# Kernel tuning notes

Measured on AMD Instinct MI355X. Metric: run time of the kernel, lower is better.

## Reference

```python
import jax, jax.numpy as jnp
import numpy as np

B, N, D, H, NDIMS, NS = 4, 1024, 512, 8, 3, 1
HD = D // H


def setup_inputs() -> dict:
    key = jax.random.key(0)
    ks = jax.random.split(key, 10)
    x = jax.random.normal(ks[0], (B, N, D), dtype=jnp.float32)
    coords = jax.random.normal(ks[1], (B, N, NDIMS), dtype=jnp.float32)
    # pad last 64 key positions in half the batch
    key_padding_mask = jnp.zeros((B, N), dtype=bool).at[: B // 2, -64:].set(True)
    s = 1.0 / np.sqrt(D)
    Wqkv = jax.random.normal(ks[2], (3 * D, D), dtype=jnp.float32) * s  # torch Linear weight [out,in]
    Wout = jax.random.normal(ks[3], (D, D), dtype=jnp.float32) * s
    bout = jnp.zeros((D,), dtype=jnp.float32)
    fin = NDIMS + 1  # num_dims>1 -> dist channel appended
    W1 = jax.random.normal(ks[4], (H * 4, fin), dtype=jnp.float32) / np.sqrt(fin)
    b1 = jnp.zeros((H * 4,), dtype=jnp.float32)
    W2 = jax.random.normal(ks[5], (H, H * 4), dtype=jnp.float32) / np.sqrt(H * 4)
    b2 = jnp.zeros((H,), dtype=jnp.float32)
    bias_alpha = jax.random.normal(ks[6], (1,), dtype=jnp.float32)
    return dict(x=x, coords=coords, key_padding_mask=key_padding_mask,
                bias_alpha=bias_alpha, W1=W1, b1=b1, W2=W2, b2=b2,
                Wqkv=Wqkv, Wout=Wout, bout=bout)


def reference(x, coords, key_padding_mask, bias_alpha, W1, b1, W2, b2, Wqkv, Wout, bout):
    scale = HD ** (-0.5)
    qkv = x @ Wqkv.T  # [B,N,3D]
    q, k, v = jnp.split(qkv, 3, axis=-1)
    q = q.reshape(B, N, H, HD).transpose(0, 2, 1, 3)  # [B,H,N,HD]
    k = k.reshape(B, N, H, HD).transpose(0, 2, 1, 3)
    v = v.reshape(B, N, H, HD).transpose(0, 2, 1, 3)

    dpos = coords[:, :, None, :] - coords[:, None, :, :]  # [B,N,N,ndims]
    dist = jnp.linalg.norm(dpos, axis=-1, keepdims=True)
    dpos = jnp.concatenate([dpos, dist], axis=-1)  # [B,N,N,ndims+1]
    h = jax.nn.gelu(dpos @ W1.T + b1, approximate=False)
    bias = (h @ W2.T + b2).transpose(0, 3, 1, 2)  # [B,H,N,N]
    # zero bias rows/cols for special tokens
    valid = jnp.arange(N) >= NS
    bias = bias * (valid[:, None] & valid[None, :])[None, None]

    dots = jnp.einsum('bhid,bhjd->bhij', q, k) * scale
    logits = dots + bias_alpha[0] * bias
    logits = jnp.where(key_padding_mask[:, None, None, :], -jnp.inf, logits)
    attn = jax.nn.softmax(logits, axis=-1)
    out = jnp.einsum('bhij,bhjd->bhid', attn, v)
    out = out.transpose(0, 2, 1, 3).reshape(B, N, D)
    return out @ Wout.T + bout, attn
```

## Files before the change

### kernel.cpp

```cpp
#include <hip/hip_runtime.h>
#include <hip/hip_fp16.h>
#include <stdint.h>
#include <math.h>

#define B_  4
#define N_  1024
#define D_  512
#define H_  8
#define HD_ 64

typedef short s16x8 __attribute__((ext_vector_type(8)));
typedef float f32x4 __attribute__((ext_vector_type(4)));
typedef float f32x2 __attribute__((ext_vector_type(2)));
typedef __fp16 f16x2 __attribute__((ext_vector_type(2)));
typedef __fp16 f16x8 __attribute__((ext_vector_type(8)));

typedef const __attribute__((address_space(1))) void* gas1p;
typedef __attribute__((address_space(3))) void* las3p;
__device__ __forceinline__ void gload16(const void* g, void* l) {
    __builtin_amdgcn_global_load_lds((gas1p)g, (las3p)l, 16, 0, 0);
}

__device__ __forceinline__ unsigned short f2bf(float f) {
    unsigned u = __float_as_uint(f);
    u += 0x7fffu + ((u >> 16) & 1u);
    return (unsigned short)(u >> 16);
}
__device__ __forceinline__ float bf2f(unsigned short h) {
    return __uint_as_float(((unsigned)h) << 16);
}

__device__ __forceinline__ float fast_gelu(float x) {
    float ax = fabsf(x) * 0.7071067811865476f;
    float t  = __builtin_amdgcn_rcpf(fmaf(0.3275911f, ax, 1.0f));
    float e  = __expf(-ax * ax);
    float poly = t * fmaf(t, fmaf(t, fmaf(t, fmaf(t, 1.061405429f, -1.453152027f),
                                          1.421413741f), -0.284496736f), 0.254829592f);
    float erfv = 1.0f - poly * e;
    float s = copysignf(erfv, x);
    return 0.5f * x * (1.0f + s);
}

__global__ void k_split(const float* __restrict__ s, unsigned short* __restrict__ h,
                        unsigned short* __restrict__ l, int n) {
    int i = blockIdx.x * 256 + threadIdx.x;
    if (i < n) {
        float x = s[i];
        unsigned short hb = f2bf(x);
        h[i] = hb;
        l[i] = f2bf(x - bf2f(hb));
    }
}

__global__ void k_mask_detect(const unsigned char* __restrict__ m, int* __restrict__ flag) {
    __shared__ int s;
    if (threadIdx.x == 0) s = 0;
    __syncthreads();
    int found = 0;
    for (int i = threadIdx.x; i < B_ * N_; i += 256)
        if ((i & 3) && m[i]) found = 1;
    if (found) atomicOr(&s, 1);
    __syncthreads();
    if (threadIdx.x == 0) flag[0] = s;
}

__global__ __launch_bounds__(256) void k_gemm3(
    const unsigned short* __restrict__ Ah, const unsigned short* __restrict__ Al,
    const unsigned short* __restrict__ Bwh, const unsigned short* __restrict__ Bwl,
    float* __restrict__ C, const float* __restrict__ bias, int M, int Nn, int K)
{
    constexpr int BM = 64, BN = 128, BK = 64;
    __shared__ unsigned short At[BM * BK];
    __shared__ unsigned short Bt[BN * BK];
    const int tid = threadIdx.x, lane = tid & 63, wid = tid >> 6;
    const int m0 = blockIdx.x * BM, n0 = blockIdx.y * BN;
    const int wm = wid >> 1, wn = wid & 1;
    f32x4 acc[2][4] = {};
    const unsigned short* Aps[3] = {Ah, Ah, Al};
    const unsigned short* Bps[3] = {Bwh, Bwl, Bwh};

    for (int combo = 0; combo < 3; ++combo) {
        const unsigned short* __restrict__ Ap = Aps[combo];
        const unsigned short* __restrict__ Bp = Bps[combo];
        for (int k0 = 0; k0 < K; k0 += BK) {
            __syncthreads();
            #pragma unroll
            for (int r = 0; r < 2; ++r) {
                int s = r * 256 + tid, row = s >> 3, c8 = s & 7;
                gload16(Ap + (size_t)(m0 + row) * K + k0 + c8 * 8, At + s * 8);
            }
            #pragma unroll
            for (int r = 0; r < 4; ++r) {
                int s = r * 256 + tid, row = s >> 3, c8 = s & 7;
                gload16(Bp + (size_t)(n0 + row) * K + k0 + c8 * 8, Bt + s * 8);
            }
            __syncthreads();
            #pragma unroll
            for (int kk = 0; kk < BK; kk += 32) {
                s16x8 a[2], bb[4];
                #pragma unroll
                for (int fm = 0; fm < 2; ++fm)
                    a[fm] = *(const s16x8*)(At + (wm * 32 + fm * 16 + (lane & 15)) * BK + kk + (lane >> 4) * 8);
                #pragma unroll
                for (int fn = 0; fn < 4; ++fn)
                    bb[fn] = *(const s16x8*)(Bt + (wn * 64 + fn * 16 + (lane & 15)) * BK + kk + (lane >> 4) * 8);
                #pragma unroll
                for (int fm = 0; fm < 2; ++fm)
                    #pragma unroll
                    for (int fn = 0; fn < 4; ++fn)
                        acc[fm][fn] = __builtin_amdgcn_mfma_f32_16x16x32_bf16(a[fm], bb[fn], acc[fm][fn], 0, 0, 0);
            }
        }
    }
    #pragma unroll
    for (int fm = 0; fm < 2; ++fm)
        #pragma unroll
        for (int fn = 0; fn < 4; ++fn)
            #pragma unroll
            for (int r = 0; r < 4; ++r) {
                int row  = m0 + wm * 32 + fm * 16 + (lane >> 4) * 4 + r;
                int coln = n0 + wn * 64 + fn * 16 + (lane & 15);
                float v = acc[fm][fn][r];
                if (bias) v += bias[coln];
                C[(size_t)row * Nn + coln] = v;
            }
}

__global__ void k_rearrange(const float* __restrict__ qkv, unsigned short* __restrict__ qp,
                            unsigned short* __restrict__ kp) {
    int t = blockIdx.x * 256 + threadIdx.x;
    int d = t & 63, n = (t >> 6) & 1023, h = (t >> 16) & 7, b = t >> 19;
    const float* src = qkv + ((size_t)(b * N_ + n)) * (3 * D_) + h * HD_ + d;
    float q = src[0], k = src[D_];
    unsigned short qh = f2bf(q), ql = f2bf(q - bf2f(qh));
    unsigned short kh = f2bf(k), kl = f2bf(k - bf2f(kh));
    size_t base = ((size_t)(b * H_ + h) * N_ + n) * 128;
    qp[base + d] = qh; qp[base + 64 + d] = ql;
    kp[base + d] = kh; kp[base + 64 + d] = kl;
}

__global__ void k_vtrans(const float* __restrict__ qkv, unsigned short* __restrict__ vT) {
    __shared__ unsigned short T[64][65];
    int n0 = blockIdx.x * 64, h = blockIdx.y, b = blockIdx.z;
    int tid = threadIdx.x;
    #pragma unroll
    for (int rep = 0; rep < 16; ++rep) {
        int idx = rep * 256 + tid;
        int nl = idx >> 6, d = idx & 63;
        T[nl][d] = f2bf(qkv[((size_t)(b * N_ + n0 + nl)) * (3 * D_) + 2 * D_ + h * HD_ + d]);
    }
    __syncthreads();
    #pragma unroll
    for (int rep = 0; rep < 16; ++rep) {
        int idx = rep * 256 + tid;
        int dl = idx >> 6, nl = idx & 63;
        vT[((size_t)(b * H_ + h) * HD_ + dl) * N_ + n0 + nl] = T[nl][dl];
    }
}

__global__ void k_nodeproj(const float* __restrict__ coords, const float* __restrict__ W1,
                           unsigned short* __restrict__ PtT) {
    int bn = blockIdx.x * 256 + threadIdx.x;
    const float* cc = coords + (size_t)bn * 3;
    float c0 = cc[0], c1 = cc[1], c2 = cc[2];
    unsigned short outv[32];
    #pragma unroll
    for (int c = 0; c < 32; ++c) {
        float v = 32.f * (W1[c * 4] * c0 + W1[c * 4 + 1] * c1 + W1[c * 4 + 2] * c2);
        __half hv = __float2half(v);
        outv[c] = *(unsigned short*)&hv;
    }
    #pragma unroll
    for (int k = 0; k < 4; ++k)
        *(s16x8*)(PtT + (size_t)bn * 32 + k * 8) = *(const s16x8*)(outv + k * 8);
}

__global__ __launch_bounds__(256) void k_bias(
    const float* __restrict__ coords, const float* __restrict__ alpha,
    const float* __restrict__ W1, const float* __restrict__ b1,
    const float* __restrict__ W2, const float* __restrict__ b2,
    const unsigned short* __restrict__ PtT,
    unsigned short* __restrict__ biasH)
{
    __shared__ unsigned short sPj[256 * 40];
    __shared__ float lut[512];
    __shared__ float SPi[32], swd32[32], sb2f[8];
    __shared__ float sdist[256];
    const int tid = threadIdx.x, lane = tid & 63, wid = tid >> 6;
    const int bid = blockIdx.x;
    const int j0 = (bid & 3) * 256;
    const int i  = (bid >> 2) & 1023;
    const int b  = bid >> 12;

    {
        float xk = (tid - 128) * 0.03125f;
        float g0 = fast_gelu(xk);
        float g1 = fast_gelu(xk + 0.03125f);
        lut[tid * 2]     = g0;
        lut[tid * 2 + 1] = g1 - g0;
    }
    if (tid < 32) {
        const float* ci = coords + ((size_t)b * N_ + i) * 3;
        float w0 = W1[tid * 4], w1 = W1[tid * 4 + 1], w2 = W1[tid * 4 + 2], w3 = W1[tid * 4 + 3];
        SPi[tid]   = 32.f * (w0 * ci[0] + w1 * ci[1] + w2 * ci[2] + b1[tid]) + 128.f;
        swd32[tid] = 32.f * w3;
    }
    if (tid < 8) sb2f[tid] = b2[tid];
    {
        const unsigned short* src = PtT + ((size_t)(b * N_) + j0) * 32;
        #pragma unroll
        for (int k = 0; k < 4; ++k) {
            int idx = k * 256 + tid;
            *(s16x8*)(sPj + (idx >> 2) * 40 + (idx & 3) * 8) = *(const s16x8*)(src + idx * 8);
        }
    }
    {
        const float* ci = coords + ((size_t)b * N_ + i) * 3;
        const float* cj = coords + ((size_t)b * N_ + j0 + tid) * 3;
        float dx = ci[0] - cj[0], dy = ci[1] - cj[1], dz = ci[2] - cj[2];
        sdist[tid] = sqrtf(dx * dx + dy * dy + dz * dz);
    }
    __syncthreads();

    const int hh = lane & 15;
    const int q  = lane >> 4;
    const float alph = alpha[0];
    const float vfi = (i >= 1) ? 1.f : 0.f;

    f16x8 bw;
    {
        int hw = hh & 7;
        #pragma unroll
        for (int e = 0; e < 8; ++e) {
            float wv = W2[hw * 32 + q * 8 + e];
            bw[e] = (hh < 8) ? (__fp16)wv : (__fp16)0.f;
        }
    }

    #pragma unroll 1
    for (int m = 0; m < 4; ++m) {
        const int pm = m * 16 + hh;
        const float dist = sdist[wid * 64 + pm];
        s16x8 praw = *(const s16x8*)(sPj + (wid * 64 + pm) * 40 + q * 8);
        f16x8 af;
        #pragma unroll
        for (int e = 0; e < 8; ++e) {
            int c = q * 8 + e;
            unsigned short u = (unsigned short)praw[e];
            float pj = __half2float(*(const __half*)&u);
            float t  = fmaf(swd32[c], dist, SPi[c] - pj);
            float tc = fminf(fmaxf(t, 0.f), 255.f);
            float fi = floorf(tc);
            int   ii = (int)fi;
            float fr = tc - fi;
            f32x2 vs = *(const f32x2*)(lut + ii * 2);
            float gg = fmaf(fr, vs[1], vs[0]);
            float xb = fmaf(t, 0.03125f, -4.f);
            gg = (t > 254.f) ? xb : gg;
            af[e] = (__fp16)gg;
        }
        f32x4 c4 = {0.f, 0.f, 0.f, 0.f};
        c4 = __builtin_amdgcn_mfma_f32_16x16x32_f16(af, bw, c4, 0, 0, 0);
        if (hh < 8) {
            const int jb = j0 + wid * 64 + m * 16 + q * 4;
            const float b2h = sb2f[hh];
            float v0 = ((jb     >= 1) ? alph : 0.f) * vfi * (c4[0] + b2h);
            float v1 = ((jb + 1 >= 1) ? alph : 0.f) * vfi * (c4[1] + b2h);
            float v2 = ((jb + 2 >= 1) ? alph : 0.f) * vfi * (c4[2] + b2h);
            float v3 = ((jb + 3 >= 1) ? alph : 0.f) * vfi * (c4[3] + b2h);
            __half h0 = __float2half(v0), h1 = __float2half(v1);
            __half h2 = __float2half(v2), h3 = __float2half(v3);
            unsigned int lo = (unsigned)*(unsigned short*)&h0 | ((unsigned)*(unsigned short*)&h1 << 16);
            unsigned int hi = (unsigned)*(unsigned short*)&h2 | ((unsigned)*(unsigned short*)&h3 << 16);
            unsigned long long pk = (unsigned long long)lo | ((unsigned long long)hi << 32);
            *(unsigned long long*)(biasH + ((size_t)(b * H_ + hh) * N_ + i) * N_ + jb) = pk;
        }
    }
}

__global__ __launch_bounds__(256, 4) void k_attn(
    const unsigned short* __restrict__ qp, const unsigned short* __restrict__ kp,
    const unsigned short* __restrict__ vT,
    const unsigned short* __restrict__ biasH,
    float* __restrict__ attnout,
    const unsigned char* __restrict__ mraw, const int* __restrict__ flag,
    unsigned short* __restrict__ avh, unsigned short* __restrict__ avl)
{
    __shared__ s16x8 pool16[2048];
    __shared__ unsigned char smask[N_];
    __shared__ float redm[16][4];
    __shared__ float reds[16][4];
    const int tid = threadIdx.x, lane = tid & 63, wid = tid >> 6;

    int flat = blockIdx.x + 64 * (blockIdx.y + 8 * blockIdx.z);
    int swz  = (flat & 7) * 256 + (flat >> 3);
    const int i0 = (swz & 63) * 16;
    const int h  = (swz >> 6) & 7;
    const int b  = swz >> 9;
    const size_t bh = (size_t)(b * H_ + h);
    const int g = lane >> 4;
    const int cl = lane & 15;

    if (flag[0] != 0) {
        for (int i2 = tid; i2 < N_; i2 += 256) smask[i2] = mraw[b * N_ + i2];
    } else {
        const int* mi = (const int*)mraw;
        for (int i2 = tid; i2 < N_; i2 += 256) smask[i2] = (unsigned char)(mi[b * N_ + i2] != 0);
    }

    const unsigned short* qrow = qp + (bh * N_ + i0 + cl) * 128 + g * 8;
    s16x8 aqh0 = *(const s16x8*)(qrow);
    s16x8 aqh1 = *(const s16x8*)(qrow + 32);
    s16x8 aql0 = *(const s16x8*)(qrow + 64);
    s16x8 aql1 = *(const s16x8*)(qrow + 96);

    int soff[4];
    #pragma unroll
    for (int p = 0; p < 4; ++p) {
        int o = p * 4096 + tid * 16;
        int row = o >> 8, offl = o & 255;
        soff[p] = row * 128 + ((offl ^ ((row & 7) << 4)) >> 1);
    }
    const unsigned short* kbase = kp + bh * (size_t)N_ * 128;

    const int lr = wid * 16 + cl;
    int rdoff[4];
    #pragma unroll
    for (int f = 0; f < 4; ++f)
        rdoff[f] = lr * 256 + ((g * 16 + f * 64) ^ ((lr & 7) << 4));

    char* poolb = (char*)pool16;

    #pragma unroll
    for (int p = 0; p < 4; ++p)
        gload16(kbase + soff[p], poolb + p * 4096 + tid * 16);
    __syncthreads();

    f32x4 acc[16];
    #pragma unroll
    for (int c = 0; c < 16; ++c) {
        if (c < 15) {
            const unsigned short* cb = kbase + (size_t)(c + 1) * 8192;
            char* wb = poolb + ((c + 1) & 1) * 16384;
            #pragma unroll
            for (int p = 0; p < 4; ++p)
                gload16(cb + soff[p], wb + p * 4096 + tid * 16);
        }
        char* kb = poolb + (c & 1) * 16384;
        s16x8 k0 = *(const s16x8*)(kb + rdoff[0]);
        s16x8 k1 = *(const s16x8*)(kb + rdoff[1]);
        s16x8 k2 = *(const s16x8*)(kb + rdoff[2]);
        s16x8 k3 = *(const s16x8*)(kb + rdoff[3]);
        f32x4 a = {0.f, 0.f, 0.f, 0.f};
        a = __builtin_amdgcn_mfma_f32_16x16x32_bf16(aqh0, k0, a, 0, 0, 0);
        a = __builtin_amdgcn_mfma_f32_16x16x32_bf16(aqh1, k1, a, 0, 0, 0);
        a = __builtin_amdgcn_mfma_f32_16x16x32_bf16(aqh0, k2, a, 0, 0, 0);
        a = __builtin_amdgcn_mfma_f32_16x16x32_bf16(aqh1, k3, a, 0, 0, 0);
        a = __builtin_amdgcn_mfma_f32_16x16x32_bf16(aql0, k0, a, 0, 0, 0);
        a = __builtin_amdgcn_mfma_f32_16x16x32_bf16(aql1, k1, a, 0, 0, 0);
        acc[c] = a;
        __syncthreads();
    }

    {
        const unsigned short* bsrc = biasH + (bh * N_ + i0) * N_;
        unsigned short* bl = (unsigned short*)poolb;
        #pragma unroll
        for (int p2 = 0; p2 < 8; ++p2) {
            int idx = p2 * 256 + tid;
            gload16(bsrc + (size_t)idx * 8, bl + idx * 8);
        }
    }
    __syncthreads();

    const float scale = 0.125f;
    const unsigned short* bl = (const unsigned short*)poolb;
    #pragma unroll
    for (int j = 0; j < 16; ++j) {
        const int col = (j * 4 + wid) * 16 + cl;
        const bool mj = (smask[col] != 0);
        #pragma unroll
        for (int r = 0; r < 4; ++r) {
            unsigned short u = bl[(g * 4 + r) * 1024 + col];
            float bv = __half2float(*(const __half*)&u);
            acc[j][r] = mj ? -1e30f : fmaf(acc[j][r], scale, bv);
        }
    }

    float m[4];
    #pragma unroll
    for (int r = 0; r < 4; ++r) {
        float mm = acc[0][r];
        #pragma unroll
        for (int j = 1; j < 16; ++j) mm = fmaxf(mm, acc[j][r]);
        m[r] = mm;
    }
    #pragma unroll
    for (int msk = 1; msk < 16; msk <<= 1)
        #pragma unroll
        for (int r = 0; r < 4; ++r) m[r] = fmaxf(m[r], __shfl_xor(m[r], msk));
    if (cl == 0)
        #pragma unroll
        for (int r = 0; r < 4; ++r) redm[g * 4 + r][wid] = m[r];
    __syncthreads();
    #pragma unroll
    for (int r = 0; r < 4; ++r) {
        int row = g * 4 + r;
        m[r] = fmaxf(fmaxf(redm[row][0], redm[row][1]), fmaxf(redm[row][2], redm[row][3]));
    }

    float s[4] = {0.f, 0.f, 0.f, 0.f};
    #pragma unroll
    for (int j = 0; j < 16; ++j)
        #pragma unroll
        for (int r = 0; r < 4; ++r) {
            float e = __expf(acc[j][r] - m[r]);
            acc[j][r] = e;
            s[r] += e;
        }
    #pragma unroll
    for (int msk = 1; msk < 16; msk <<= 1)
        #pragma unroll
        for (int r = 0; r < 4; ++r) s[r] += __shfl_xor(s[r], msk);
    if (cl == 0)
        #pragma unroll
        for (int r = 0; r < 4; ++r) reds[g * 4 + r][wid] = s[r];
    __syncthreads();
    float sinv[4];
    #pragma unroll
    for (int r = 0; r < 4; ++r) {
        int row = g * 4 + r;
        sinv[r] = 1.0f / (reds[row][0] + reds[row][1] + reds[row][2] + reds[row][3]);
    }

    float* gattn = attnout + (bh * N_ + i0) * N_;
    char* Pb = poolb;
    #pragma unroll
    for (int j = 0; j < 16; ++j) {
        const int col = (j * 4 + wid) * 16 + cl;
        #pragma unroll
        for (int r = 0; r < 4; ++r) {
            const int row = g * 4 + r;
            float e = acc[j][r];
            __builtin_nontemporal_store(e * sinv[r], &gattn[(size_t)row * N_ + col]);
            int byte = row * 2048 + ((col * 2) ^ ((row & 7) << 4));
            *(unsigned short*)(Pb + byte) = f2bf(e);
        }
    }
    __syncthreads();

    {
        const int d0 = wid * 16;
        f32x4 acc2 = {0.f, 0.f, 0.f, 0.f};
        const unsigned short* vrow = vT + (bh * HD_ + d0 + cl) * N_ + g * 8;
        const int rowA = cl;
        const int swzb = (rowA & 7) << 4;
        for (int kk = 0; kk < N_; kk += 32) {
            s16x8 bfrag = *(const s16x8*)(vrow + kk);
            int byte = rowA * 2048 + (((kk + g * 8) * 2) ^ swzb);
            s16x8 af = *(const s16x8*)(Pb + byte);
            acc2 = __builtin_amdgcn_mfma_f32_16x16x32_bf16(af, bfrag, acc2, 0, 0, 0);
        }
        #pragma unroll
        for (int r = 0; r < 4; ++r) {
            const int row = g * 4 + r;
            const int dd = d0 + cl;
            float v = acc2[r] * sinv[r];
            unsigned short hv = f2bf(v);
            size_t o = ((size_t)(b * N_) + i0 + row) * D_ + h * HD_ + dd;
            avh[o] = hv;
            avl[o] = f2bf(v - bf2f(hv));
        }
    }
}

extern "C" void kernel_launch(void* const* d_in, const int* in_sizes, int n_in,
                              void* d_out, int out_size, void* d_ws, size_t ws_size,
                              hipStream_t stream) {
    (void)in_sizes; (void)n_in; (void)out_size; (void)ws_size;
    const float* x      = (const float*)d_in[0];
    const float* coords = (const float*)d_in[1];
    const unsigned char* kpm = (const unsigned char*)d_in[2];
    const float* alpha  = (const float*)d_in[3];
    const float* W1     = (const float*)d_in[4];
    const float* b1     = (const float*)d_in[5];
    const float* W2     = (const float*)d_in[6];
    const float* b2     = (const float*)d_in[7];
    const float* Wqkv   = (const float*)d_in[8];
    const float* Wout   = (const float*)d_in[9];
    const float* bout   = (const float*)d_in[10];

    float* out  = (float*)d_out;
    float* attn = out + (size_t)B_ * N_ * D_;

    char* w = (char*)d_ws;
    auto alloc = [&](size_t bytes) { char* p = w; w += (bytes + 255) & ~(size_t)255; return p; };
    const size_t SZ_X  = (size_t)B_ * N_ * D_;
    const size_t SZ_WQ = (size_t)3 * D_ * D_;
    const size_t SZ_WO = (size_t)D_ * D_;

    unsigned short* wo_hi = (unsigned short*)alloc(SZ_WO * 2);
    unsigned short* wo_lo = (unsigned short*)alloc(SZ_WO * 2);
    unsigned short* qp = (unsigned short*)alloc((size_t)B_ * H_ * N_ * 128 * 2);
    unsigned short* kp = (unsigned short*)alloc((size_t)B_ * H_ * N_ * 128 * 2);
    unsigned short* vT = (unsigned short*)alloc((size_t)B_ * H_ * HD_ * N_ * 2);
    unsigned short* av_hi = (unsigned short*)alloc(SZ_X * 2);
    unsigned short* av_lo = (unsigned short*)alloc(SZ_X * 2);
    unsigned short* PtT = (unsigned short*)alloc((size_t)B_ * N_ * 32 * 2);
    int* flag = (int*)alloc(256);

    char* uni = (char*)alloc(0);
    unsigned short* x_hi = (unsigned short*)uni;
    unsigned short* x_lo = x_hi + SZ_X;
    unsigned short* wq_hi = x_lo + SZ_X;
    unsigned short* wq_lo = wq_hi + SZ_WQ;
    float* qkv = (float*)(wq_lo + SZ_WQ);
    unsigned short* biasH = (unsigned short*)uni;

    k_split<<<(int)((SZ_X + 255) / 256), 256, 0, stream>>>(x, x_hi, x_lo, (int)SZ_X);
    k_split<<<(int)((SZ_WQ + 255) / 256), 256, 0, stream>>>(Wqkv, wq_hi, wq_lo, (int)SZ_WQ);
    k_split<<<(int)((SZ_WO + 255) / 256), 256, 0, stream>>>(Wout, wo_hi, wo_lo, (int)SZ_WO);
    k_mask_detect<<<1, 256, 0, stream>>>(kpm, flag);
    k_nodeproj<<<(B_ * N_) / 256, 256, 0, stream>>>(coords, W1, PtT);
    k_gemm3<<<dim3(64, 12), 256, 0, stream>>>(x_hi, x_lo, wq_hi, wq_lo, qkv, nullptr,
                                              B_ * N_, 3 * D_, D_);
    k_rearrange<<<(B_ * H_ * N_ * HD_) / 256, 256, 0, stream>>>(qkv, qp, kp);
    k_vtrans<<<dim3(16, H_, B_), 256, 0, stream>>>(qkv, vT);
    k_bias<<<(B_ * N_ * N_) / 256, 256, 0, stream>>>(coords, alpha, W1, b1, W2, b2, PtT, biasH);
    k_attn<<<dim3(64, H_, B_), 256, 0, stream>>>(qp, kp, vT, biasH, attn, kpm, flag, av_hi, av_lo);
    k_gemm3<<<dim3(64, 4), 256, 0, stream>>>(av_hi, av_lo, wo_hi, wo_lo, out, bout,
                                             B_ * N_, D_, D_);
}
```

Measured before the change: 236.0 us.

## Process 32 query rows per attention block to reuse K tiles

The attention kernel now handles 32 query rows per block instead of 16. Each K chunk staged in shared memory feeds two sets of MFMAs, so K traffic from global memory is halved and the grid shrinks to 1024 blocks. The cost is twice the accumulator registers (acc[32]), twice the shared memory, and launch bounds lowered to 2 blocks per CU. Occupancy and latency hiding may drop.

```diff
diff --git a/kernel.cpp b/kernel.cpp
--- a/kernel.cpp
+++ b/kernel.cpp
@@ -278,7 +278,7 @@
     }
 }
 
-__global__ __launch_bounds__(256, 4) void k_attn(
+__global__ __launch_bounds__(256, 2) void k_attn(
     const unsigned short* __restrict__ qp, const unsigned short* __restrict__ kp,
     const unsigned short* __restrict__ vT,
     const unsigned short* __restrict__ biasH,
@@ -286,17 +286,17 @@
     const unsigned char* __restrict__ mraw, const int* __restrict__ flag,
     unsigned short* __restrict__ avh, unsigned short* __restrict__ avl)
 {
-    __shared__ s16x8 pool16[2048];
+    __shared__ s16x8 pool16[4096];
     __shared__ unsigned char smask[N_];
-    __shared__ float redm[16][4];
-    __shared__ float reds[16][4];
+    __shared__ float redm[32][4];
+    __shared__ float reds[32][4];
     const int tid = threadIdx.x, lane = tid & 63, wid = tid >> 6;
 
-    int flat = blockIdx.x + 64 * (blockIdx.y + 8 * blockIdx.z);
-    int swz  = (flat & 7) * 256 + (flat >> 3);
-    const int i0 = (swz & 63) * 16;
-    const int h  = (swz >> 6) & 7;
-    const int b  = swz >> 9;
+    int flat = blockIdx.x + 32 * (blockIdx.y + 8 * blockIdx.z);
+    int swz  = (flat & 7) * 128 + (flat >> 3);
+    const int i0 = (swz & 31) * 32;
+    const int h  = (swz >> 5) & 7;
+    const int b  = swz >> 8;
     const size_t bh = (size_t)(b * H_ + h);
     const int g = lane >> 4;
     const int cl = lane & 15;
@@ -308,11 +308,16 @@
         for (int i2 = tid; i2 < N_; i2 += 256) smask[i2] = (unsigned char)(mi[b * N_ + i2] != 0);
     }
 
-    const unsigned short* qrow = qp + (bh * N_ + i0 + cl) * 128 + g * 8;
-    s16x8 aqh0 = *(const s16x8*)(qrow);
-    s16x8 aqh1 = *(const s16x8*)(qrow + 32);
-    s16x8 aql0 = *(const s16x8*)(qrow + 64);
-    s16x8 aql1 = *(const s16x8*)(qrow + 96);
+    const unsigned short* qr0 = qp + (bh * N_ + i0 + cl) * 128 + g * 8;
+    const unsigned short* qr1 = qp + (bh * N_ + i0 + 16 + cl) * 128 + g * 8;
+    s16x8 aqh0_0 = *(const s16x8*)(qr0);
+    s16x8 aqh1_0 = *(const s16x8*)(qr0 + 32);
+    s16x8 aql0_0 = *(const s16x8*)(qr0 + 64);
+    s16x8 aql1_0 = *(const s16x8*)(qr0 + 96);
+    s16x8 aqh0_1 = *(const s16x8*)(qr1);
+    s16x8 aqh1_1 = *(const s16x8*)(qr1 + 32);
+    s16x8 aql0_1 = *(const s16x8*)(qr1 + 64);
+    s16x8 aql1_1 = *(const s16x8*)(qr1 + 96);
 
     int soff[4];
     #pragma unroll
@@ -336,7 +341,7 @@
         gload16(kbase + soff[p], poolb + p * 4096 + tid * 16);
     __syncthreads();
 
-    f32x4 acc[16];
+    f32x4 acc[32];
     #pragma unroll
     for (int c = 0; c < 16; ++c) {
         if (c < 15) {
@@ -352,13 +357,21 @@
         s16x8 k2 = *(const s16x8*)(kb + rdoff[2]);
         s16x8 k3 = *(const s16x8*)(kb + rdoff[3]);
         f32x4 a = {0.f, 0.f, 0.f, 0.f};
-        a = __builtin_amdgcn_mfma_f32_16x16x32_bf16(aqh0, k0, a, 0, 0, 0);
-        a = __builtin_amdgcn_mfma_f32_16x16x32_bf16(aqh1, k1, a, 0, 0, 0);
-        a = __builtin_amdgcn_mfma_f32_16x16x32_bf16(aqh0, k2, a, 0, 0, 0);
-        a = __builtin_amdgcn_mfma_f32_16x16x32_bf16(aqh1, k3, a, 0, 0, 0);
-        a = __builtin_amdgcn_mfma_f32_16x16x32_bf16(aql0, k0, a, 0, 0, 0);
-        a = __builtin_amdgcn_mfma_f32_16x16x32_bf16(aql1, k1, a, 0, 0, 0);
+        a = __builtin_amdgcn_mfma_f32_16x16x32_bf16(aqh0_0, k0, a, 0, 0, 0);
+        a = __builtin_amdgcn_mfma_f32_16x16x32_bf16(aqh1_0, k1, a, 0, 0, 0);
+        a = __builtin_amdgcn_mfma_f32_16x16x32_bf16(aqh0_0, k2, a, 0, 0, 0);
+        a = __builtin_amdgcn_mfma_f32_16x16x32_bf16(aqh1_0, k3, a, 0, 0, 0);
+        a = __builtin_amdgcn_mfma_f32_16x16x32_bf16(aql0_0, k0, a, 0, 0, 0);
+        a = __builtin_amdgcn_mfma_f32_16x16x32_bf16(aql1_0, k1, a, 0, 0, 0);
         acc[c] = a;
+        f32x4 a2 = {0.f, 0.f, 0.f, 0.f};
+        a2 = __builtin_amdgcn_mfma_f32_16x16x32_bf16(aqh0_1, k0, a2, 0, 0, 0);
+        a2 = __builtin_amdgcn_mfma_f32_16x16x32_bf16(aqh1_1, k1, a2, 0, 0, 0);
+        a2 = __builtin_amdgcn_mfma_f32_16x16x32_bf16(aqh0_1, k2, a2, 0, 0, 0);
+        a2 = __builtin_amdgcn_mfma_f32_16x16x32_bf16(aqh1_1, k3, a2, 0, 0, 0);
+        a2 = __builtin_amdgcn_mfma_f32_16x16x32_bf16(aql0_1, k0, a2, 0, 0, 0);
+        a2 = __builtin_amdgcn_mfma_f32_16x16x32_bf16(aql1_1, k1, a2, 0, 0, 0);
+        acc[16 + c] = a2;
         __syncthreads();
     }
 
@@ -366,7 +379,7 @@
         const unsigned short* bsrc = biasH + (bh * N_ + i0) * N_;
         unsigned short* bl = (unsigned short*)poolb;
         #pragma unroll
-        for (int p2 = 0; p2 < 8; ++p2) {
+        for (int p2 = 0; p2 < 16; ++p2) {
             int idx = p2 * 256 + tid;
             gload16(bsrc + (size_t)idx * 8, bl + idx * 8);
         }
@@ -381,56 +394,79 @@
         const bool mj = (smask[col] != 0);
         #pragma unroll
         for (int r = 0; r < 4; ++r) {
-            unsigned short u = bl[(g * 4 + r) * 1024 + col];
-            float bv = __half2float(*(const __half*)&u);
-            acc[j][r] = mj ? -1e30f : fmaf(acc[j][r], scale, bv);
-        }
-    }
-
-    float m[4];
+            int row0 = g * 4 + r;
+            unsigned short u0 = bl[row0 * 1024 + col];
+            float bv0 = __half2float(*(const __half*)&u0);
+            acc[j][r] = mj ? -1e30f : fmaf(acc[j][r], scale, bv0);
+            int row1 = 16 + row0;
+            unsigned short u1 = bl[row1 * 1024 + col];
+            float bv1 = __half2float(*(const __half*)&u1);
+            acc[16 + j][r] = mj ? -1e30f : fmaf(acc[16 + j][r], scale, bv1);
+        }
+    }
+
+    float m0[4], m1[4];
     #pragma unroll
     for (int r = 0; r < 4; ++r) {
-        float mm = acc[0][r];
-        #pragma unroll
-        for (int j = 1; j < 16; ++j) mm = fmaxf(mm, acc[j][r]);
-        m[r] = mm;
+        float a = acc[0][r], c2 = acc[16][r];
+        #pragma unroll
+        for (int j = 1; j < 16; ++j) { a = fmaxf(a, acc[j][r]); c2 = fmaxf(c2, acc[16 + j][r]); }
+        m0[r] = a; m1[r] = c2;
     }
     #pragma unroll
     for (int msk = 1; msk < 16; msk <<= 1)
         #pragma unroll
-        for (int r = 0; r < 4; ++r) m[r] = fmaxf(m[r], __shfl_xor(m[r], msk));
+        for (int r = 0; r < 4; ++r) {
+            m0[r] = fmaxf(m0[r], __shfl_xor(m0[r], msk));
+            m1[r] = fmaxf(m1[r], __shfl_xor(m1[r], msk));
+        }
     if (cl == 0)
         #pragma unroll
-        for (int r = 0; r < 4; ++r) redm[g * 4 + r][wid] = m[r];
+        for (int r = 0; r < 4; ++r) {
+            redm[g * 4 + r][wid] = m0[r];
+            redm[16 + g * 4 + r][wid] = m1[r];
+        }
     __syncthreads();
     #pragma unroll
     for (int r = 0; r < 4; ++r) {
         int row = g * 4 + r;
-        m[r] = fmaxf(fmaxf(redm[row][0], redm[row][1]), fmaxf(redm[row][2], redm[row][3]));
-    }
-
-    float s[4] = {0.f, 0.f, 0.f, 0.f};
+        m0[r] = fmaxf(fmaxf(redm[row][0], redm[row][1]), fmaxf(redm[row][2], redm[row][3]));
+        m1[r] = fmaxf(fmaxf(redm[16 + row][0], redm[16 + row][1]),
+                      fmaxf(redm[16 + row][2], redm[16 + row][3]));
+    }
+
+    float s0[4] = {0.f, 0.f, 0.f, 0.f};
+    float s1[4] = {0.f, 0.f, 0.f, 0.f};
     #pragma unroll
     for (int j = 0; j < 16; ++j)
         #pragma unroll
         for (int r = 0; r < 4; ++r) {
-            float e = __expf(acc[j][r] - m[r]);
-            acc[j][r] = e;
-            s[r] += e;
+            float e0 = __expf(acc[j][r] - m0[r]);
+            acc[j][r] = e0; s0[r] += e0;
+            float e1 = __expf(acc[16 + j][r] - m1[r]);
+            acc[16 + j][r] = e1; s1[r] += e1;
         }
     #pragma unroll
     for (int msk = 1; msk < 16; msk <<= 1)
         #pragma unroll
-        for (int r = 0; r < 4; ++r) s[r] += __shfl_xor(s[r], msk);
+        for (int r = 0; r < 4; ++r) {
+            s0[r] += __shfl_xor(s0[r], msk);
+            s1[r] += __shfl_xor(s1[r], msk);
+        }
     if (cl == 0)
         #pragma unroll
-        for (int r = 0; r < 4; ++r) reds[g * 4 + r][wid] = s[r];
-    __syncthreads();
-    float sinv[4];
+        for (int r = 0; r < 4; ++r) {
+            reds[g * 4 + r][wid] = s0[r];
+            reds[16 + g * 4 + r][wid] = s1[r];
+        }
+    __syncthreads();
+    float sinv0[4], sinv1[4];
     #pragma unroll
     for (int r = 0; r < 4; ++r) {
         int row = g * 4 + r;
-        sinv[r] = 1.0f / (reds[row][0] + reds[row][1] + reds[row][2] + reds[row][3]);
+        sinv0[r] = 1.0f / (reds[row][0] + reds[row][1] + reds[row][2] + reds[row][3]);
+        sinv1[r] = 1.0f / (reds[16 + row][0] + reds[16 + row][1] +
+                           reds[16 + row][2] + reds[16 + row][3]);
     }
 
     float* gattn = attnout + (bh * N_ + i0) * N_;
@@ -440,20 +476,26 @@
         const int col = (j * 4 + wid) * 16 + cl;
         #pragma unroll
         for (int r = 0; r < 4; ++r) {
-            const int row = g * 4 + r;
-            float e = acc[j][r];
-            __builtin_nontemporal_store(e * sinv[r], &gattn[(size_t)row * N_ + col]);
-            int byte = row * 2048 + ((col * 2) ^ ((row & 7) << 4));
-            *(unsigned short*)(Pb + byte) = f2bf(e);
-        }
-    }
-    __syncthreads();
-
-    {
+            const int row0 = g * 4 + r;
+            float e0 = acc[j][r];
+            __builtin_nontemporal_store(e0 * sinv0[r], &gattn[(size_t)row0 * N_ + col]);
+            int byte0 = row0 * 2048 + ((col * 2) ^ ((row0 & 7) << 4));
+            *(unsigned short*)(Pb + byte0) = f2bf(e0);
+            const int row1 = 16 + row0;
+            float e1 = acc[16 + j][r];
+            __builtin_nontemporal_store(e1 * sinv1[r], &gattn[(size_t)row1 * N_ + col]);
+            int byte1 = row1 * 2048 + ((col * 2) ^ ((row1 & 7) << 4));
+            *(unsigned short*)(Pb + byte1) = f2bf(e1);
+        }
+    }
+    __syncthreads();
+
+    #pragma unroll 1
+    for (int half = 0; half < 2; ++half) {
         const int d0 = wid * 16;
         f32x4 acc2 = {0.f, 0.f, 0.f, 0.f};
         const unsigned short* vrow = vT + (bh * HD_ + d0 + cl) * N_ + g * 8;
-        const int rowA = cl;
+        const int rowA = half * 16 + cl;
         const int swzb = (rowA & 7) << 4;
         for (int kk = 0; kk < N_; kk += 32) {
             s16x8 bfrag = *(const s16x8*)(vrow + kk);
@@ -461,11 +503,12 @@
             s16x8 af = *(const s16x8*)(Pb + byte);
             acc2 = __builtin_amdgcn_mfma_f32_16x16x32_bf16(af, bfrag, acc2, 0, 0, 0);
         }
-        #pragma unroll
-        for (int r = 0; r < 4; ++r) {
-            const int row = g * 4 + r;
+        const float* sv = half ? sinv1 : sinv0;
+        #pragma unroll
+        for (int r = 0; r < 4; ++r) {
+            const int row = half * 16 + g * 4 + r;
             const int dd = d0 + cl;
-            float v = acc2[r] * sinv[r];
+            float v = acc2[r] * sv[r];
             unsigned short hv = f2bf(v);
             size_t o = ((size_t)(b * N_) + i0 + row) * D_ + h * HD_ + dd;
             avh[o] = hv;
@@ -527,7 +570,7 @@
     k_rearrange<<<(B_ * H_ * N_ * HD_) / 256, 256, 0, stream>>>(qkv, qp, kp);
     k_vtrans<<<dim3(16, H_, B_), 256, 0, stream>>>(qkv, vT);
     k_bias<<<(B_ * N_ * N_) / 256, 256, 0, stream>>>(coords, alpha, W1, b1, W2, b2, PtT, biasH);
-    k_attn<<<dim3(64, H_, B_), 256, 0, stream>>>(qp, kp, vT, biasH, attn, kpm, flag, av_hi, av_lo);
+    k_attn<<<dim3(32, H_, B_), 256, 0, stream>>>(qp, kp, vT, biasH, attn, kpm, flag, av_hi, av_lo);
     k_gemm3<<<dim3(64, 4), 256, 0, stream>>>(av_hi, av_lo, wo_hi, wo_lo, out, bout,
                                              B_ * N_, D_, D_);
 }
```

After: 239.5 us. No clear change (+1.5%).
